# Kernel tuning notes

Hardware: AMD Instinct MI355X
Metric: run time of the kernel (lower is better)

Reference implementation:

```python
import jax, jax.numpy as jnp
import numpy as np

D = 1024      # model dimension
H = 16        # heads
DK = D // H   # head dim
DFF = 4096    # ffn hidden
B, S = 2, 2048
EPS = 1e-6
NEG_SLOPE = 0.01  # torch LeakyReLU default


def setup_inputs() -> dict:
    key = jax.random.key(0)
    ks = jax.random.split(key, 12)
    sd = 1.0 / np.sqrt(D)
    sf = 1.0 / np.sqrt(DFF)
    return {
        "x": jax.random.normal(ks[0], (B, S, D), dtype=jnp.float32),
        "wq": jax.random.uniform(ks[1], (D, D), jnp.float32, -sd, sd),
        "bq": jnp.zeros((D,), jnp.float32),
        "wk": jax.random.uniform(ks[2], (D, D), jnp.float32, -sd, sd),
        "bk": jnp.zeros((D,), jnp.float32),
        "wv": jax.random.uniform(ks[3], (D, D), jnp.float32, -sd, sd),
        "bv": jnp.zeros((D,), jnp.float32),
        "wo": jax.random.uniform(ks[4], (D, D), jnp.float32, -sd, sd),
        "bo": jnp.zeros((D,), jnp.float32),
        "g1": jnp.ones((D,), jnp.float32),
        "b1": jnp.zeros((D,), jnp.float32),
        "w_ff1": jax.random.uniform(ks[5], (D, DFF), jnp.float32, -sd, sd),
        "b_ff1": jnp.zeros((DFF,), jnp.float32),
        "w_ff2": jax.random.uniform(ks[6], (DFF, D), jnp.float32, -sf, sf),
        "b_ff2": jnp.zeros((D,), jnp.float32),
        "g2": jnp.ones((D,), jnp.float32),
        "b2": jnp.zeros((D,), jnp.float32),
    }


def _layernorm(x, g, b):
    mu = jnp.mean(x, axis=-1, keepdims=True)
    var = jnp.mean(jnp.square(x - mu), axis=-1, keepdims=True)
    return (x - mu) * jax.lax.rsqrt(var + EPS) * g + b


def reference(x, wq, bq, wk, bk, wv, bv, wo, bo, g1, b1,
              w_ff1, b_ff1, w_ff2, b_ff2, g2, b2):
    # Multi-head attention
    q = (x @ wq + bq).reshape(B, S, H, DK).transpose(0, 2, 1, 3)  # [B,H,S,DK]
    k = (x @ wk + bk).reshape(B, S, H, DK).transpose(0, 2, 1, 3)
    v = (x @ wv + bv).reshape(B, S, H, DK).transpose(0, 2, 1, 3)
    scores = jnp.einsum('bhqd,bhkd->bhqk', q, k) / np.sqrt(DK)
    attn = jax.nn.softmax(scores, axis=-1)
    ctx = jnp.einsum('bhqk,bhkd->bhqd', attn, v)
    ctx = ctx.transpose(0, 2, 1, 3).reshape(B, S, D)
    attn_out = ctx @ wo + bo
    # residual + LN1 (dropout = identity in eval)
    h = _layernorm(attn_out + x, g1, b1)
    # FFN with LeakyReLU
    ff = jnp.where(h @ w_ff1 + b_ff1 > 0,
                   h @ w_ff1 + b_ff1,
                   NEG_SLOPE * (h @ w_ff1 + b_ff1))
    ff = ff @ w_ff2 + b_ff2
    return _layernorm(ff + h, g2, b2)
```

## Files before the change

### kernel.cpp

```cpp
#include <hip/hip_runtime.h>
#include <math.h>

#define D_MODEL 1024
#define NHEAD   16
#define DKH     64
#define DFF_    4096
#define BB      2
#define SS      2048
#define MTOT    (BB*SS)
#define EPSLN   1e-6f
#define NEG_SLOPE 0.01f

typedef unsigned short u16;
typedef unsigned int   u32;
typedef __bf16 bf16x8 __attribute__((ext_vector_type(8)));
typedef float  f32x4  __attribute__((ext_vector_type(4)));
typedef u16    u16x4  __attribute__((ext_vector_type(4)));

__device__ __forceinline__ u16 f2bf(float f) {
    u32 u = __float_as_uint(f);
    u = (u + 0x7fffu + ((u >> 16) & 1u)) >> 16;
    return (u16)u;
}
__device__ __forceinline__ float bf2f(u16 u) {
    return __uint_as_float(((u32)u) << 16);
}

__device__ __forceinline__ void gload_lds16(const u16* g, u16* l) {
    __builtin_amdgcn_global_load_lds(
        (const __attribute__((address_space(1))) u32*)g,
        (__attribute__((address_space(3))) u32*)l,
        16, 0, 0);
}

__device__ __forceinline__ void transpose_tile(const float* __restrict__ W,
        u16* __restrict__ WT, int N, int out_stride, int out_row_off,
        float scale, int bx, int by, u16* T)
{
    const int t  = threadIdx.x;
    const int n0 = bx * 64;
    const int k0 = by * 64;
    #pragma unroll
    for (int i = 0; i < 4; ++i) {
        int r = i * 16 + (t >> 4);
        int c = (t & 15) * 4;
        float4 v = *(const float4*)&W[(size_t)(k0 + r) * N + n0 + c];
        T[(c + 0) * 72 + r] = f2bf(v.x * scale);
        T[(c + 1) * 72 + r] = f2bf(v.y * scale);
        T[(c + 2) * 72 + r] = f2bf(v.z * scale);
        T[(c + 3) * 72 + r] = f2bf(v.w * scale);
    }
    __syncthreads();
    #pragma unroll
    for (int i = 0; i < 4; ++i) {
        int nr = i * 16 + (t >> 4);
        int kc = (t & 15) * 4;
        u16x4 o = { T[nr*72 + kc], T[nr*72 + kc + 1], T[nr*72 + kc + 2], T[nr*72 + kc + 3] };
        *(u16x4*)&WT[(size_t)(out_row_off + n0 + nr) * out_stride + k0 + kc] = o;
    }
}

__global__ __launch_bounds__(256)
void prep(const float* __restrict__ x, u16* __restrict__ x_bf,
          const float* __restrict__ wq, const float* __restrict__ wk,
          const float* __restrict__ wv, const float* __restrict__ wo,
          const float* __restrict__ wff1, const float* __restrict__ wff2,
          u16* __restrict__ wqkvT, u16* __restrict__ woT,
          u16* __restrict__ wff1T, u16* __restrict__ wff2T,
          const float* __restrict__ bq, const float* __restrict__ bk,
          const float* __restrict__ bv, float* __restrict__ qkv_bias,
          float qscale)
{
    __shared__ u16 T[64 * 72];
    int blk = blockIdx.x;
    if (blk < 4096) {
        int i = blk * 256 + threadIdx.x;
        float4 v = ((const float4*)x)[i];
        u16x4 o = { f2bf(v.x), f2bf(v.y), f2bf(v.z), f2bf(v.w) };
        ((u16x4*)x_bf)[i] = o;
        return;
    }
    blk -= 4096;
    if (blk < 1024) {
        int which = blk >> 8, r = blk & 255;
        const float* Ws = which == 0 ? wq : which == 1 ? wk : which == 2 ? wv : wo;
        u16* Wd   = which == 3 ? woT : wqkvT;
        int off   = which == 3 ? 0 : which * 1024;
        float sc  = which == 0 ? qscale : 1.0f;
        transpose_tile(Ws, Wd, 1024, 1024, off, sc, r & 15, r >> 4, T);
        return;
    }
    blk -= 1024;
    if (blk < 1024) {
        transpose_tile(wff1, wff1T, 4096, 1024, 0, 1.0f, blk & 63, blk >> 6, T);
        return;
    }
    blk -= 1024;
    if (blk < 1024) {
        transpose_tile(wff2, wff2T, 1024, 4096, 0, 1.0f, blk & 15, blk >> 4, T);
        return;
    }
    blk -= 1024;
    int i = blk * 256 + threadIdx.x;
    qkv_bias[i] = (i < 1024) ? bq[i] * qscale
                : (i < 2048) ? bk[i - 1024] : bv[i - 2048];
}

template<int EPI>
__global__ __launch_bounds__(256)
void gemm_bf16(const u16* __restrict__ A, const u16* __restrict__ BT,
               const float* __restrict__ bias, void* __restrict__ Cout,
               u16* __restrict__ Vt, int M, int N, int k_len, int kstride)
{
    __shared__ u16 As[128 * 64];
    __shared__ u16 Bs[128 * 64];
    const int tid  = threadIdx.x;
    const int w    = tid >> 6;
    const int lane = tid & 63;
    const int lm   = lane & 15;
    const int lq   = lane >> 4;
    const int row0 = blockIdx.y * 128;
    const int col0 = blockIdx.x * 128;
    const int k_off = blockIdx.z * k_len;
    const int wrow = (w >> 1) * 64;
    const int wcol = (w & 1) * 64;

    f32x4 acc[4][4] = {};

    const int r_i = lane >> 3;
    const int csw = ((lane & 7) ^ r_i) * 8;
    const u16* a_src = A  + (size_t)(row0 + w * 32 + r_i) * kstride + k_off + csw;
    const u16* b_src = BT + (size_t)(col0 + w * 32 + r_i) * kstride + k_off + csw;
    u16* a_dst = &As[(w * 32) * 64];
    u16* b_dst = &Bs[(w * 32) * 64];

    const int fr0 = (lq ^ (lm & 7)) * 8;
    const int fr1 = ((4 + lq) ^ (lm & 7)) * 8;
    const u16* a_rd = &As[(wrow + lm) * 64];
    const u16* b_rd = &Bs[(wcol + lm) * 64];

    for (int k0 = 0; k0 < k_len; k0 += 64) {
        #pragma unroll
        for (int i = 0; i < 4; ++i) {
            gload_lds16(a_src + k0 + (size_t)(i * 8) * kstride, a_dst + (i * 8) * 64);
            gload_lds16(b_src + k0 + (size_t)(i * 8) * kstride, b_dst + (i * 8) * 64);
        }
        __syncthreads();
        #pragma unroll
        for (int h = 0; h < 2; ++h) {
            const int fo = h ? fr1 : fr0;
            bf16x8 av[4], bv[4];
            #pragma unroll
            for (int m = 0; m < 4; ++m) av[m] = *(const bf16x8*)(a_rd + m * 16 * 64 + fo);
            #pragma unroll
            for (int n = 0; n < 4; ++n) bv[n] = *(const bf16x8*)(b_rd + n * 16 * 64 + fo);
            #pragma unroll
            for (int m = 0; m < 4; ++m)
                #pragma unroll
                for (int n = 0; n < 4; ++n)
                    acc[m][n] = __builtin_amdgcn_mfma_f32_16x16x32_bf16(av[m], bv[n], acc[m][n], 0, 0, 0);
        }
        __syncthreads();
    }

    float bz[4] = {0.f, 0.f, 0.f, 0.f};
    if (EPI != 3) {
        #pragma unroll
        for (int n = 0; n < 4; ++n) bz[n] = bias[col0 + wcol + n * 16 + lm];
    }

    if (EPI == 4 && col0 >= 2048) {
        #pragma unroll
        for (int m = 0; m < 4; ++m) {
            int rbase = row0 + wrow + m * 16 + lq * 4;
            int b = rbase >> 11, s = rbase & 2047;
            #pragma unroll
            for (int n = 0; n < 4; ++n) {
                int c = col0 + wcol + n * 16 + lm - 2048;
                u16x4 pk = { f2bf(acc[m][n][0] + bz[n]), f2bf(acc[m][n][1] + bz[n]),
                             f2bf(acc[m][n][2] + bz[n]), f2bf(acc[m][n][3] + bz[n]) };
                *(u16x4*)&Vt[(size_t)((b * 16 + (c >> 6)) * 64 + (c & 63)) * 2048 + s] = pk;
            }
        }
        return;
    }

    u16* Cz = (u16*)Cout + (EPI == 3 ? (size_t)blockIdx.z * M * N : 0);
    #pragma unroll
    for (int m = 0; m < 4; ++m) {
        #pragma unroll
        for (int e = 0; e < 4; ++e) {
            int row = row0 + wrow + m * 16 + lq * 4 + e;
            #pragma unroll
            for (int n = 0; n < 4; ++n) {
                int col = col0 + wcol + n * 16 + lm;
                float v = acc[m][n][e] + bz[n];
                if (EPI == 1) v = v > 0.f ? v : NEG_SLOPE * v;
                Cz[(size_t)row * N + col] = f2bf(v);
            }
        }
    }
}

__global__ __launch_bounds__(256)
void attn_mfma(const u16* __restrict__ QKV, const u16* __restrict__ Vt,
               u16* __restrict__ ctx)
{
    __shared__ u16 QP[64 * 64];
    __shared__ u16 Kb[2][64 * 64];
    __shared__ u16 Vb[2][64 * 64];
    const int tid = threadIdx.x, w = tid >> 6, lane = tid & 63;
    const int lm = lane & 15, lq = lane >> 4;
    const int q0 = blockIdx.x * 64;
    const int bh = blockIdx.y;
    const int b  = bh >> 4, h = bh & 15;
    const size_t row_b = (size_t)b * SS;
    const int ccol = h * DKH;

    const int r_i = lane >> 3;
    const int csw = ((lane & 7) ^ r_i) * 8;
    const u16* ksrc = QKV + (row_b + w * 16 + r_i) * 3072 + 1024 + ccol + csw;
    const u16* vsrc = Vt + ((size_t)bh * 64 + w * 16 + r_i) * SS + csw;
    const u16* qsrc = QKV + (row_b + q0 + w * 16 + r_i) * 3072 + ccol + csw;

    gload_lds16(qsrc,                    &QP[(w * 16) * 64]);
    gload_lds16(qsrc + (size_t)8 * 3072, &QP[(w * 16 + 8) * 64]);
    #pragma unroll
    for (int i = 0; i < 2; ++i) {
        gload_lds16(ksrc + (size_t)(i * 8) * 3072, &Kb[0][(w * 16 + i * 8) * 64]);
        gload_lds16(vsrc + (size_t)(i * 8) * SS,   &Vb[0][(w * 16 + i * 8) * 64]);
    }
    __syncthreads();

    const int fr0 = (lq ^ (lm & 7)) * 8;
    const int fr1 = ((4 + lq) ^ (lm & 7)) * 8;
    bf16x8 aq0 = *(const bf16x8*)&QP[(w * 16 + lm) * 64 + fr0];
    bf16x8 aq1 = *(const bf16x8*)&QP[(w * 16 + lm) * 64 + fr1];
    __syncthreads();

    bf16x8 ones;
    #pragma unroll
    for (int j = 0; j < 8; ++j) ones[j] = (__bf16)1.0f;

    f32x4 o[4] = {};
    f32x4 lacc = {};

    for (int kt = 0; kt < SS / 64; ++kt) {
        const int cur = kt & 1;
        if (kt < SS / 64 - 1) {
            const int nxt = cur ^ 1;
            const size_t koff = (size_t)(kt + 1) * 64;
            #pragma unroll
            for (int i = 0; i < 2; ++i) {
                gload_lds16(ksrc + (koff + i * 8) * 3072, &Kb[nxt][(w * 16 + i * 8) * 64]);
                gload_lds16(vsrc + koff + (size_t)(i * 8) * SS, &Vb[nxt][(w * 16 + i * 8) * 64]);
            }
        }
        f32x4 s[4] = {};
        #pragma unroll
        for (int n = 0; n < 4; ++n) {
            bf16x8 bk0 = *(const bf16x8*)&Kb[cur][(n * 16 + lm) * 64 + fr0];
            bf16x8 bk1 = *(const bf16x8*)&Kb[cur][(n * 16 + lm) * 64 + fr1];
            s[n] = __builtin_amdgcn_mfma_f32_16x16x32_bf16(aq0, bk0, s[n], 0, 0, 0);
            s[n] = __builtin_amdgcn_mfma_f32_16x16x32_bf16(aq1, bk1, s[n], 0, 0, 0);
        }
        const int rb = lq * 4;
        const int cw = lm & 7;
        #pragma unroll
        for (int n = 0; n < 4; ++n) {
            const int cb = n * 2 + (lm >> 3);
            #pragma unroll
            for (int e = 0; e < 4; ++e) {
                float p = __builtin_exp2f(s[n][e]);
                const int row = w * 16 + rb + e;
                QP[row * 64 + ((cb ^ ((rb + e) & 7)) * 8) + cw] =
                    (u16)((__float_as_uint(p) + 0x8000u) >> 16);
            }
        }
        bf16x8 ap0 = *(const bf16x8*)&QP[(w * 16 + lm) * 64 + fr0];
        bf16x8 ap1 = *(const bf16x8*)&QP[(w * 16 + lm) * 64 + fr1];
        #pragma unroll
        for (int n = 0; n < 4; ++n) {
            bf16x8 bv0 = *(const bf16x8*)&Vb[cur][(n * 16 + lm) * 64 + fr0];
            bf16x8 bv1 = *(const bf16x8*)&Vb[cur][(n * 16 + lm) * 64 + fr1];
            o[n] = __builtin_amdgcn_mfma_f32_16x16x32_bf16(ap0, bv0, o[n], 0, 0, 0);
            o[n] = __builtin_amdgcn_mfma_f32_16x16x32_bf16(ap1, bv1, o[n], 0, 0, 0);
        }
        lacc = __builtin_amdgcn_mfma_f32_16x16x32_bf16(ap0, ones, lacc, 0, 0, 0);
        lacc = __builtin_amdgcn_mfma_f32_16x16x32_bf16(ap1, ones, lacc, 0, 0, 0);
        __syncthreads();
    }

    #pragma unroll
    for (int e = 0; e < 4; ++e) {
        float inv = 1.0f / lacc[e];
        int row = q0 + w * 16 + lq * 4 + e;
        u16* dst = ctx + (row_b + row) * D_MODEL + ccol;
        #pragma unroll
        for (int n = 0; n < 4; ++n)
            dst[n * 16 + lm] = f2bf(o[n][e] * inv);
    }
}

template<int OUTF32, int RESBF>
__global__ __launch_bounds__(256)
void add_ln(const u16* __restrict__ C0, const u16* __restrict__ C1,
            const float* __restrict__ cbias, const void* __restrict__ resid,
            const float* __restrict__ g, const float* __restrict__ beta,
            float* __restrict__ outf, u16* __restrict__ outb)
{
    __shared__ float red[8];
    const int row = blockIdx.x;
    const int tid = threadIdx.x;
    u16x4 p0 = ((const u16x4*)(C0 + (size_t)row * D_MODEL))[tid];
    u16x4 p1 = ((const u16x4*)(C1 + (size_t)row * D_MODEL))[tid];
    float4 cb = ((const float4*)cbias)[tid];
    float4 rr;
    if (RESBF) {
        u16x4 rb = ((const u16x4*)((const u16*)resid + (size_t)row * D_MODEL))[tid];
        rr = { bf2f(rb.x), bf2f(rb.y), bf2f(rb.z), bf2f(rb.w) };
    } else {
        rr = ((const float4*)((const float*)resid + (size_t)row * D_MODEL))[tid];
    }
    float4 v = { bf2f(p0.x) + bf2f(p1.x) + cb.x + rr.x,
                 bf2f(p0.y) + bf2f(p1.y) + cb.y + rr.y,
                 bf2f(p0.z) + bf2f(p1.z) + cb.z + rr.z,
                 bf2f(p0.w) + bf2f(p1.w) + cb.w + rr.w };
    float s  = v.x + v.y + v.z + v.w;
    float sq = v.x*v.x + v.y*v.y + v.z*v.z + v.w*v.w;
    #pragma unroll
    for (int off = 32; off > 0; off >>= 1) {
        s  += __shfl_down(s,  off, 64);
        sq += __shfl_down(sq, off, 64);
    }
    const int wv = tid >> 6;
    if ((tid & 63) == 0) { red[wv] = s; red[4 + wv] = sq; }
    __syncthreads();
    float st  = red[0] + red[1] + red[2] + red[3];
    float sqt = red[4] + red[5] + red[6] + red[7];
    float mu   = st * (1.0f / D_MODEL);
    float var  = sqt * (1.0f / D_MODEL) - mu * mu;
    float rstd = rsqrtf(var + EPSLN);
    float4 gv = ((const float4*)g)[tid];
    float4 bt = ((const float4*)beta)[tid];
    float4 ov;
    ov.x = (v.x - mu) * rstd * gv.x + bt.x;
    ov.y = (v.y - mu) * rstd * gv.y + bt.y;
    ov.z = (v.z - mu) * rstd * gv.z + bt.z;
    ov.w = (v.w - mu) * rstd * gv.w + bt.w;
    if (OUTF32) {
        ((float4*)(outf + (size_t)row * D_MODEL))[tid] = ov;
    } else {
        u16x4 ob = { f2bf(ov.x), f2bf(ov.y), f2bf(ov.z), f2bf(ov.w) };
        ((u16x4*)(outb + (size_t)row * D_MODEL))[tid] = ob;
    }
}

extern "C" void kernel_launch(void* const* d_in, const int* in_sizes, int n_in,
                              void* d_out, int out_size, void* d_ws, size_t ws_size,
                              hipStream_t stream) {
    const float* x     = (const float*)d_in[0];
    const float* wq    = (const float*)d_in[1];
    const float* bq    = (const float*)d_in[2];
    const float* wk    = (const float*)d_in[3];
    const float* bk    = (const float*)d_in[4];
    const float* wv    = (const float*)d_in[5];
    const float* bv    = (const float*)d_in[6];
    const float* wo    = (const float*)d_in[7];
    const float* bo    = (const float*)d_in[8];
    const float* g1    = (const float*)d_in[9];
    const float* b1    = (const float*)d_in[10];
    const float* w_ff1 = (const float*)d_in[11];
    const float* b_ff1 = (const float*)d_in[12];
    const float* w_ff2 = (const float*)d_in[13];
    const float* b_ff2 = (const float*)d_in[14];
    const float* g2    = (const float*)d_in[15];
    const float* b2    = (const float*)d_in[16];
    float* out = (float*)d_out;

    const float qscale = 0.18033688011112042f;

    char* W = (char*)d_ws;
    u16*   x_bf    = (u16*)(W + 0);
    u16*   wqkvT   = (u16*)(W + 8388608);
    u16*   woT     = (u16*)(W + 14680064);
    u16*   wff1T   = (u16*)(W + 16777216);
    u16*   wff2T   = (u16*)(W + 25165824);
    u16*   QKV     = (u16*)(W + 33554432);
    u16*   VtG     = (u16*)(W + 58720256);
    u16*   C0      = (u16*)(W + 67108864);
    u16*   C1      = (u16*)(W + 75497472);
    u16*   h_bf    = (u16*)(W + 83886080);
    float* qkv_bias= (float*)(W + 92274688);
    u16*   ctx     = x_bf;
    u16*   ff1_bf  = QKV;

    dim3 blk(256);
    prep<<<7180, blk, 0, stream>>>(x, x_bf, wq, wk, wv, wo, w_ff1, w_ff2,
                                   wqkvT, woT, wff1T, wff2T,
                                   bq, bk, bv, qkv_bias, qscale);
    gemm_bf16<4><<<dim3(24, 32, 1), blk, 0, stream>>>(x_bf, wqkvT, qkv_bias, QKV, VtG, MTOT, 3072, 1024, 1024);
    attn_mfma<<<dim3(32, 32), blk, 0, stream>>>(QKV, VtG, ctx);
    gemm_bf16<3><<<dim3(8, 32, 2), blk, 0, stream>>>(ctx, woT, nullptr, C0, nullptr, MTOT, 1024, 512, 1024);
    add_ln<0, 0><<<MTOT, blk, 0, stream>>>(C0, C1, bo, x, g1, b1, nullptr, h_bf);
    gemm_bf16<1><<<dim3(32, 32, 1), blk, 0, stream>>>(h_bf, wff1T, b_ff1, ff1_bf, nullptr, MTOT, DFF_, 1024, 1024);
    gemm_bf16<3><<<dim3(8, 32, 2), blk, 0, stream>>>(ff1_bf, wff2T, nullptr, C0, nullptr, MTOT, 1024, 2048, 4096);
    add_ln<1, 1><<<MTOT, blk, 0, stream>>>(C0, C1, b_ff2, h_bf, g2, b2, out, nullptr);
}
```

Before: 362.5 us.

## Double attention query tile to 128 rows per block and transpose PV MFMA

Each attention block now handles 128 query rows, 32 per wave, instead of 64. Every K/V tile staged in LDS is therefore reused across twice as many queries, which halves K/V global traffic and the number of block-level syncs per query. The PV product is reordered so V is the A operand and P the B operand, which lets the output be stored as packed 4-element vectors. In exchange the grid shrinks to 512 blocks, which may underfill the GPU's compute units, and register and LDS use per block go up.

```diff
diff --git a/kernel.cpp b/kernel.cpp
--- a/kernel.cpp
+++ b/kernel.cpp
@@ -206,12 +206,12 @@
 void attn_mfma(const u16* __restrict__ QKV, const u16* __restrict__ Vt,
                u16* __restrict__ ctx)
 {
-    __shared__ u16 QP[64 * 64];
+    __shared__ u16 QP[128 * 64];
     __shared__ u16 Kb[2][64 * 64];
     __shared__ u16 Vb[2][64 * 64];
     const int tid = threadIdx.x, w = tid >> 6, lane = tid & 63;
     const int lm = lane & 15, lq = lane >> 4;
-    const int q0 = blockIdx.x * 64;
+    const int q0 = blockIdx.x * 128;
     const int bh = blockIdx.y;
     const int b  = bh >> 4, h = bh & 15;
     const size_t row_b = (size_t)b * SS;
@@ -221,10 +221,11 @@
     const int csw = ((lane & 7) ^ r_i) * 8;
     const u16* ksrc = QKV + (row_b + w * 16 + r_i) * 3072 + 1024 + ccol + csw;
     const u16* vsrc = Vt + ((size_t)bh * 64 + w * 16 + r_i) * SS + csw;
-    const u16* qsrc = QKV + (row_b + q0 + w * 16 + r_i) * 3072 + ccol + csw;
-
-    gload_lds16(qsrc,                    &QP[(w * 16) * 64]);
-    gload_lds16(qsrc + (size_t)8 * 3072, &QP[(w * 16 + 8) * 64]);
+    const u16* qsrc = QKV + (row_b + q0 + w * 32 + r_i) * 3072 + ccol + csw;
+
+    #pragma unroll
+    for (int i = 0; i < 4; ++i)
+        gload_lds16(qsrc + (size_t)(i * 8) * 3072, &QP[(w * 32 + i * 8) * 64]);
     #pragma unroll
     for (int i = 0; i < 2; ++i) {
         gload_lds16(ksrc + (size_t)(i * 8) * 3072, &Kb[0][(w * 16 + i * 8) * 64]);
@@ -234,16 +235,20 @@
 
     const int fr0 = (lq ^ (lm & 7)) * 8;
     const int fr1 = ((4 + lq) ^ (lm & 7)) * 8;
-    bf16x8 aq0 = *(const bf16x8*)&QP[(w * 16 + lm) * 64 + fr0];
-    bf16x8 aq1 = *(const bf16x8*)&QP[(w * 16 + lm) * 64 + fr1];
+    bf16x8 aq[2][2];
+    #pragma unroll
+    for (int m = 0; m < 2; ++m) {
+        aq[m][0] = *(const bf16x8*)&QP[(w * 32 + m * 16 + lm) * 64 + fr0];
+        aq[m][1] = *(const bf16x8*)&QP[(w * 32 + m * 16 + lm) * 64 + fr1];
+    }
     __syncthreads();
 
     bf16x8 ones;
     #pragma unroll
     for (int j = 0; j < 8; ++j) ones[j] = (__bf16)1.0f;
 
-    f32x4 o[4] = {};
-    f32x4 lacc = {};
+    f32x4 o[4][2] = {};
+    f32x4 lacc[2] = {};
 
     for (int kt = 0; kt < SS / 64; ++kt) {
         const int cur = kt & 1;
@@ -256,49 +261,68 @@
                 gload_lds16(vsrc + koff + (size_t)(i * 8) * SS, &Vb[nxt][(w * 16 + i * 8) * 64]);
             }
         }
-        f32x4 s[4] = {};
+        f32x4 s[2][4] = {};
         #pragma unroll
         for (int n = 0; n < 4; ++n) {
             bf16x8 bk0 = *(const bf16x8*)&Kb[cur][(n * 16 + lm) * 64 + fr0];
             bf16x8 bk1 = *(const bf16x8*)&Kb[cur][(n * 16 + lm) * 64 + fr1];
-            s[n] = __builtin_amdgcn_mfma_f32_16x16x32_bf16(aq0, bk0, s[n], 0, 0, 0);
-            s[n] = __builtin_amdgcn_mfma_f32_16x16x32_bf16(aq1, bk1, s[n], 0, 0, 0);
+            #pragma unroll
+            for (int m = 0; m < 2; ++m) {
+                s[m][n] = __builtin_amdgcn_mfma_f32_16x16x32_bf16(aq[m][0], bk0, s[m][n], 0, 0, 0);
+                s[m][n] = __builtin_amdgcn_mfma_f32_16x16x32_bf16(aq[m][1], bk1, s[m][n], 0, 0, 0);
+            }
         }
         const int rb = lq * 4;
         const int cw = lm & 7;
         #pragma unroll
-        for (int n = 0; n < 4; ++n) {
-            const int cb = n * 2 + (lm >> 3);
-            #pragma unroll
-            for (int e = 0; e < 4; ++e) {
-                float p = __builtin_exp2f(s[n][e]);
-                const int row = w * 16 + rb + e;
-                QP[row * 64 + ((cb ^ ((rb + e) & 7)) * 8) + cw] =
-                    (u16)((__float_as_uint(p) + 0x8000u) >> 16);
-            }
-        }
-        bf16x8 ap0 = *(const bf16x8*)&QP[(w * 16 + lm) * 64 + fr0];
-        bf16x8 ap1 = *(const bf16x8*)&QP[(w * 16 + lm) * 64 + fr1];
-        #pragma unroll
-        for (int n = 0; n < 4; ++n) {
-            bf16x8 bv0 = *(const bf16x8*)&Vb[cur][(n * 16 + lm) * 64 + fr0];
-            bf16x8 bv1 = *(const bf16x8*)&Vb[cur][(n * 16 + lm) * 64 + fr1];
-            o[n] = __builtin_amdgcn_mfma_f32_16x16x32_bf16(ap0, bv0, o[n], 0, 0, 0);
-            o[n] = __builtin_amdgcn_mfma_f32_16x16x32_bf16(ap1, bv1, o[n], 0, 0, 0);
-        }
-        lacc = __builtin_amdgcn_mfma_f32_16x16x32_bf16(ap0, ones, lacc, 0, 0, 0);
-        lacc = __builtin_amdgcn_mfma_f32_16x16x32_bf16(ap1, ones, lacc, 0, 0, 0);
+        for (int m = 0; m < 2; ++m) {
+            #pragma unroll
+            for (int n = 0; n < 4; ++n) {
+                const int cb = n * 2 + (lm >> 3);
+                #pragma unroll
+                for (int e = 0; e < 4; ++e) {
+                    float p = __builtin_exp2f(s[m][n][e]);
+                    const int row = w * 32 + m * 16 + rb + e;
+                    QP[row * 64 + ((cb ^ ((rb + e) & 7)) * 8) + cw] =
+                        (u16)((__float_as_uint(p) + 0x8000u) >> 16);
+                }
+            }
+        }
+        bf16x8 ap[2][2];
+        #pragma unroll
+        for (int qn = 0; qn < 2; ++qn) {
+            ap[qn][0] = *(const bf16x8*)&QP[(w * 32 + qn * 16 + lm) * 64 + fr0];
+            ap[qn][1] = *(const bf16x8*)&QP[(w * 32 + qn * 16 + lm) * 64 + fr1];
+        }
+        #pragma unroll
+        for (int dm = 0; dm < 4; ++dm) {
+            bf16x8 av0 = *(const bf16x8*)&Vb[cur][(dm * 16 + lm) * 64 + fr0];
+            bf16x8 av1 = *(const bf16x8*)&Vb[cur][(dm * 16 + lm) * 64 + fr1];
+            #pragma unroll
+            for (int qn = 0; qn < 2; ++qn) {
+                o[dm][qn] = __builtin_amdgcn_mfma_f32_16x16x32_bf16(av0, ap[qn][0], o[dm][qn], 0, 0, 0);
+                o[dm][qn] = __builtin_amdgcn_mfma_f32_16x16x32_bf16(av1, ap[qn][1], o[dm][qn], 0, 0, 0);
+            }
+        }
+        #pragma unroll
+        for (int qn = 0; qn < 2; ++qn) {
+            lacc[qn] = __builtin_amdgcn_mfma_f32_16x16x32_bf16(ones, ap[qn][0], lacc[qn], 0, 0, 0);
+            lacc[qn] = __builtin_amdgcn_mfma_f32_16x16x32_bf16(ones, ap[qn][1], lacc[qn], 0, 0, 0);
+        }
         __syncthreads();
     }
 
     #pragma unroll
-    for (int e = 0; e < 4; ++e) {
-        float inv = 1.0f / lacc[e];
-        int row = q0 + w * 16 + lq * 4 + e;
-        u16* dst = ctx + (row_b + row) * D_MODEL + ccol;
-        #pragma unroll
-        for (int n = 0; n < 4; ++n)
-            dst[n * 16 + lm] = f2bf(o[n][e] * inv);
+    for (int qn = 0; qn < 2; ++qn) {
+        float inv = 1.0f / lacc[qn][0];
+        int qrow = q0 + w * 32 + qn * 16 + lm;
+        u16* dst = ctx + (row_b + qrow) * D_MODEL + ccol + lq * 4;
+        #pragma unroll
+        for (int dm = 0; dm < 4; ++dm) {
+            u16x4 pk = { f2bf(o[dm][qn][0] * inv), f2bf(o[dm][qn][1] * inv),
+                         f2bf(o[dm][qn][2] * inv), f2bf(o[dm][qn][3] * inv) };
+            *(u16x4*)&dst[dm * 16] = pk;
+        }
     }
 }
 
@@ -400,7 +424,7 @@
                                    wqkvT, woT, wff1T, wff2T,
                                    bq, bk, bv, qkv_bias, qscale);
     gemm_bf16<4><<<dim3(24, 32, 1), blk, 0, stream>>>(x_bf, wqkvT, qkv_bias, QKV, VtG, MTOT, 3072, 1024, 1024);
-    attn_mfma<<<dim3(32, 32), blk, 0, stream>>>(QKV, VtG, ctx);
+    attn_mfma<<<dim3(16, 32), blk, 0, stream>>>(QKV, VtG, ctx);
     gemm_bf16<3><<<dim3(8, 32, 2), blk, 0, stream>>>(ctx, woT, nullptr, C0, nullptr, MTOT, 1024, 512, 1024);
     add_ln<0, 0><<<MTOT, blk, 0, stream>>>(C0, C1, bo, x, g1, b1, nullptr, h_bf);
     gemm_bf16<1><<<dim3(32, 32, 1), blk, 0, stream>>>(h_bf, wff1T, b_ff1, ff1_bf, nullptr, MTOT, DFF_, 1024, 1024);
```

Result: slower. 369.9 us (+2.0%).
